# Performance work log

Measured on AMD Instinct MI355X. Metric: run time of the kernel, lower is better.

Reference implementation:

```python
import jax, jax.numpy as jnp
import numpy as np

B, T, E, H = 4, 1024, 512, 8


def setup_inputs() -> dict:
    key = jax.random.key(0)
    ks = jax.random.split(key, 8)
    s = 1.0 / np.sqrt(E)
    return {
        "x": jax.random.normal(ks[0], (B, T, E), dtype=jnp.float32),
        "mask": jnp.zeros((B, T, T), dtype=jnp.float32),
        "Wk": jax.random.uniform(ks[1], (H * E, E), minval=-s, maxval=s, dtype=jnp.float32),
        "Wq": jax.random.uniform(ks[2], (H * E, E), minval=-s, maxval=s, dtype=jnp.float32),
        "Wv": jax.random.uniform(ks[3], (H * E, E), minval=-s, maxval=s, dtype=jnp.float32),
        "Wu": jax.random.uniform(ks[4], (E, H * E), minval=-s, maxval=s, dtype=jnp.float32),
        "bu": jnp.zeros((E,), dtype=jnp.float32),
        "heads": H,
    }


def reference(x, mask, Wk, Wq, Wv, Wu, bu, heads):
    b, t, e = x.shape
    h = heads
    # Projections: torch Linear computes x @ W.T; output features laid out as [h, e]
    k = (x @ Wk.T).reshape(b, t, h, e).transpose(0, 2, 1, 3)  # [b,h,t,e]
    q = (x @ Wq.T).reshape(b, t, h, e).transpose(0, 2, 1, 3)
    v = (x @ Wv.T).reshape(b, t, h, e).transpose(0, 2, 1, 3)
    dot = jnp.einsum("bhqe,bhke->bhqk", q, k) / jnp.sqrt(jnp.float32(e))
    # mask repeat_interleave over b*h == broadcast over heads; subtracted additively
    att = jax.nn.softmax(dot - mask[:, None, :, :], axis=-1)
    out = jnp.einsum("bhqk,bhke->bhqe", att, v)  # [b,h,t,e]
    out = out.transpose(0, 2, 1, 3).reshape(b, t, h * e)
    return out @ Wu.T + bu
```

## Files before the change

kernel.cpp:

```cpp
#include <hip/hip_runtime.h>
#include <hip/hip_bf16.h>


typedef short bf16x8 __attribute__((ext_vector_type(8)));
typedef float f32x4 __attribute__((ext_vector_type(4)));
typedef unsigned short u16x8 __attribute__((ext_vector_type(8)));

__device__ __forceinline__ unsigned short f2bf(float f) {
  unsigned int u = __float_as_uint(f);
  u += 0x7FFFu + ((u >> 16) & 1u);
  return (unsigned short)(u >> 16);
}
__device__ __forceinline__ float bf2f(unsigned short s) {
  return __uint_as_float(((unsigned int)s) << 16);
}

typedef const __attribute__((address_space(1))) unsigned int* gas1_t;
typedef __attribute__((address_space(3))) unsigned int* las3_t;

__device__ __forceinline__ void gload16(const unsigned short* g, unsigned short* l) {
  __builtin_amdgcn_global_load_lds((gas1_t)g, (las3_t)l, 16, 0, 0);
}

__device__ __forceinline__ void store_val(unsigned short* p, float v) { *p = f2bf(v); }
__device__ __forceinline__ void store_val(float* p, float v) { *p = v; }

template<typename OutT>
__global__ __launch_bounds__(512, 1) void gemm_bt2(
    const unsigned short* __restrict__ A, const unsigned short* __restrict__ B,
    OutT* __restrict__ C,
    int K, int lda, int ldb, int ldc, int zshift,
    long long sAb, long long sAh, long long sBb, long long sBh,
    long long sCb, long long sCh, float alpha,
    const unsigned short* __restrict__ A2, const unsigned short* __restrict__ B2,
    OutT* __restrict__ C2, int lda2,
    long long sA2h, long long sB2h, long long sC2h, int selGE)
{
  const int tid  = threadIdx.x;
  const int lane = tid & 63;
  const int wave = tid >> 6;
  const int l15 = lane & 15, lhi = lane >> 4;
  const int wm = wave >> 2, wn = wave & 3;

  const int nx = gridDim.x, nxy = gridDim.x * gridDim.y;
  const int nwg = nxy * gridDim.z;
  int flat = blockIdx.x + nx * blockIdx.y + nxy * blockIdx.z;
  flat = (flat & 7) * (nwg >> 3) + (flat >> 3);
  const int bz = flat / nxy;
  const int rem = flat - bz * nxy;
  const int by = rem / nx;
  const int bx = rem - by * nx;

  const int bb = bz >> zshift, hh = bz & ((1 << zshift) - 1);
  const long long m0 = (long long)by * 256;
  const long long n0 = (long long)bx * 256;

  const unsigned short* Ab;
  const unsigned short* Bb;
  OutT* Cb;
  int ldaU = lda;
  if (selGE >= 0 && hh >= selGE) {
    const int h2 = hh - selGE;
    Ab = A2 + (size_t)h2 * sA2h;
    Bb = B2 + (size_t)h2 * sB2h;
    Cb = C2 + (size_t)h2 * sC2h;
    ldaU = lda2;
  } else {
    Ab = A + bb * sAb + hh * sAh;
    Bb = B + bb * sBb + hh * sBh;
    Cb = C + bb * sCb + hh * sCh;
  }

  __shared__ __align__(16) unsigned short lds[49152];

  const unsigned short* gA[2];
  const unsigned short* gB[2];
  int fidx[2];
#pragma unroll
  for (int c = 0; c < 2; ++c) {
    const int f = c * 8 + wave;
    fidx[c] = f;
    gA[c] = Ab + (size_t)(m0 + f * 16 + l15) * ldaU + lhi * 8;
    gB[c] = Bb + (size_t)(n0 + f * 16 + l15) * ldb + lhi * 8;
  }

  auto stage = [&](int n, int p) {
    unsigned short* dst = lds + p * 16384;
    const int ko = n * 32;
#pragma unroll
    for (int c = 0; c < 2; ++c) {
      gload16(gA[c] + ko, dst + fidx[c] * 512);
      gload16(gB[c] + ko, dst + 8192 + fidx[c] * 512);
    }
  };

  f32x4 acc[8][4];
#pragma unroll
  for (int m = 0; m < 8; ++m)
#pragma unroll
    for (int n = 0; n < 4; ++n) acc[m][n] = (f32x4){0.f, 0.f, 0.f, 0.f};

  const int nt = K >> 5;
  stage(0, 0);
  stage(1, 1);
  asm volatile("s_waitcnt vmcnt(4)" ::: "memory");
  __builtin_amdgcn_sched_barrier(0);
  __builtin_amdgcn_s_barrier();

  for (int t = 0; t < nt; ++t) {
    const bool pref = (t + 2 < nt);
    if (pref) stage(t + 2, (t + 2) % 3);
    const unsigned short* base = lds + (t % 3) * 16384;
    bf16x8 af[8], bf[4];
#pragma unroll
    for (int mf = 0; mf < 8; ++mf)
      af[mf] = *(const bf16x8*)(base + (wm * 8 + mf) * 512 + lane * 8);
#pragma unroll
    for (int nf = 0; nf < 4; ++nf)
      bf[nf] = *(const bf16x8*)(base + 8192 + (wn * 4 + nf) * 512 + lane * 8);
    __builtin_amdgcn_s_setprio(1);
#pragma unroll
    for (int mf = 0; mf < 8; ++mf)
#pragma unroll
      for (int nf = 0; nf < 4; ++nf)
        acc[mf][nf] = __builtin_amdgcn_mfma_f32_16x16x32_bf16(af[mf], bf[nf], acc[mf][nf], 0, 0, 0);
    __builtin_amdgcn_s_setprio(0);
    if (pref) asm volatile("s_waitcnt vmcnt(4)" ::: "memory");
    else      asm volatile("s_waitcnt vmcnt(0)" ::: "memory");
    __builtin_amdgcn_sched_barrier(0);
    __builtin_amdgcn_s_barrier();
    __builtin_amdgcn_sched_barrier(0);
  }

#pragma unroll
  for (int mf = 0; mf < 8; ++mf) {
#pragma unroll
    for (int nf = 0; nf < 4; ++nf) {
      const long long col = n0 + wn * 64 + nf * 16 + l15;
#pragma unroll
      for (int r = 0; r < 4; ++r) {
        const long long row = m0 + wm * 128 + mf * 16 + lhi * 4 + r;
        store_val(Cb + (size_t)row * ldc + col, acc[mf][nf][r] * alpha);
      }
    }
  }
}

__global__ __launch_bounds__(256) void wtrans_kernel(
    const unsigned short* __restrict__ Wq, const unsigned short* __restrict__ Wk,
    const unsigned short* __restrict__ Wv,
    unsigned short* __restrict__ Wqt, unsigned short* __restrict__ Wkt,
    unsigned short* __restrict__ Wvt)
{
  __shared__ unsigned short t[64][72];
  const int k0 = blockIdx.x * 64;
  const int i0 = blockIdx.y * 64;
  const int hz = blockIdx.z;
  const int h = hz & 7;
  const int w = hz >> 3;
  const unsigned short* src = (w == 0) ? Wq : ((w == 1) ? Wk : Wv);
  unsigned short* dst = (w == 0) ? Wqt : ((w == 1) ? Wkt : Wvt);
  const int tid = threadIdx.x;
  const int r = tid >> 2, c16 = (tid & 3) * 16;
  const unsigned short* sp = src + (size_t)(h * 512 + k0 + r) * 512 + i0 + c16;
  u16x8 v0 = *(const u16x8*)sp;
  u16x8 v1 = *(const u16x8*)(sp + 8);
#pragma unroll
  for (int j = 0; j < 8; ++j) { t[r][c16 + j] = v0[j]; t[r][c16 + 8 + j] = v1[j]; }
  __syncthreads();
  unsigned short o[16];
#pragma unroll
  for (int j = 0; j < 16; ++j) o[j] = t[c16 + j][r];
  unsigned short* dp = dst + (size_t)h * 262144 + (size_t)(i0 + r) * 512 + k0 + c16;
  *(u16x8*)dp = *(u16x8*)o;
  *(u16x8*)(dp + 8) = *(u16x8*)(o + 8);
}

__global__ __launch_bounds__(256) void reduce_kernel(
    const float* __restrict__ P, const float* __restrict__ bias,
    float* __restrict__ out)
{
  const int i = blockIdx.x * 256 + threadIdx.x;
  const int col4 = i & 127;
  const float4* p4 = (const float4*)P + i;
  float4 s = p4[0];
#pragma unroll
  for (int z = 1; z < 8; ++z) {
    float4 v = p4[(size_t)z * 524288];
    s.x += v.x; s.y += v.y; s.z += v.z; s.w += v.w;
  }
  float4 b = ((const float4*)bias)[col4];
  s.x += b.x; s.y += b.y; s.z += b.z; s.w += b.w;
  ((float4*)out)[i] = s;
}

__global__ __launch_bounds__(256) void cast5_kernel(
    const float* __restrict__ s0, const float* __restrict__ s1,
    const float* __restrict__ s2, const float* __restrict__ s3,
    const float* __restrict__ s4, unsigned short* __restrict__ dst)
{
  const int seg = blockIdx.x >> 11;
  const int off = (blockIdx.x & 2047) * 256 + threadIdx.x;
  const float* s = s0;
  if (seg == 1) s = s1; else if (seg == 2) s = s2;
  else if (seg == 3) s = s3; else if (seg == 4) s = s4;
  float4 v = ((const float4*)s)[off];
  ushort4 o;
  o.x = f2bf(v.x); o.y = f2bf(v.y); o.z = f2bf(v.z); o.w = f2bf(v.w);
  ((ushort4*)dst)[(size_t)seg * 524288 + off] = o;
}

__global__ __launch_bounds__(256) void softmax_kernel(
    unsigned short* __restrict__ S, const float* __restrict__ mask)
{
  const int wave = threadIdx.x >> 6;
  const int lane = threadIdx.x & 63;
  const long long row = (long long)blockIdx.x * 4 + wave;
  const int q = (int)(row & 1023);
  const int b = (int)(row >> 13);
  unsigned short* Srow = S + row * 1024;
  const float* mrow = mask + ((size_t)b * 1024 + q) * 1024;

  u16x8 sv0 = ((const u16x8*)Srow)[lane * 2];
  u16x8 sv1 = ((const u16x8*)Srow)[lane * 2 + 1];
  float mk[16];
  const float4* m4 = (const float4*)mrow + lane * 4;
#pragma unroll
  for (int t = 0; t < 4; ++t) {
    float4 v = m4[t];
    mk[t * 4 + 0] = v.x; mk[t * 4 + 1] = v.y; mk[t * 4 + 2] = v.z; mk[t * 4 + 3] = v.w;
  }

  float lg[16];
#pragma unroll
  for (int j = 0; j < 8; ++j) lg[j] = bf2f(sv0[j]) - mk[j];
#pragma unroll
  for (int j = 0; j < 8; ++j) lg[8 + j] = bf2f(sv1[j]) - mk[8 + j];

  float mx = lg[0];
#pragma unroll
  for (int j = 1; j < 16; ++j) mx = fmaxf(mx, lg[j]);
#pragma unroll
  for (int off = 32; off > 0; off >>= 1) mx = fmaxf(mx, __shfl_xor(mx, off));

  float ex[16], sm = 0.f;
#pragma unroll
  for (int j = 0; j < 16; ++j) { ex[j] = __expf(lg[j] - mx); sm += ex[j]; }
#pragma unroll
  for (int off = 32; off > 0; off >>= 1) sm += __shfl_xor(sm, off);
  const float rinv = 1.0f / sm;

  u16x8 o0, o1;
#pragma unroll
  for (int j = 0; j < 8; ++j) o0[j] = f2bf(ex[j] * rinv);
#pragma unroll
  for (int j = 0; j < 8; ++j) o1[j] = f2bf(ex[8 + j] * rinv);
  ((u16x8*)Srow)[lane * 2] = o0;
  ((u16x8*)Srow)[lane * 2 + 1] = o1;
}

extern "C" void kernel_launch(void* const* d_in, const int* in_sizes, int n_in,
                              void* d_out, int out_size, void* d_ws, size_t ws_size,
                              hipStream_t stream) {
  const float* x    = (const float*)d_in[0];
  const float* mask = (const float*)d_in[1];
  const float* Wk   = (const float*)d_in[2];
  const float* Wq   = (const float*)d_in[3];
  const float* Wv   = (const float*)d_in[4];
  const float* Wu   = (const float*)d_in[5];
  const float* bu   = (const float*)d_in[6];

  const size_t MB = 1024 * 1024;
  if (ws_size < 192 * MB) return;
  char* ws = (char*)d_ws;
  unsigned short* xb  = (unsigned short*)(ws + 0 * MB);
  unsigned short* Wqb = (unsigned short*)(ws + 4 * MB);
  unsigned short* Wkb = (unsigned short*)(ws + 8 * MB);
  unsigned short* Wvb = (unsigned short*)(ws + 12 * MB);
  unsigned short* Wub = (unsigned short*)(ws + 16 * MB);
  unsigned short* Wqt = (unsigned short*)(ws + 20 * MB);
  unsigned short* Wkt = (unsigned short*)(ws + 24 * MB);
  unsigned short* Wvt = (unsigned short*)(ws + 28 * MB);
  unsigned short* Nh  = (unsigned short*)(ws + 32 * MB);
  unsigned short* Gh  = (unsigned short*)(ws + 36 * MB);
  unsigned short* xM  = (unsigned short*)(ws + 40 * MB);
  unsigned short* xGt = (unsigned short*)(ws + 72 * MB);
  unsigned short* Sb  = (unsigned short*)(ws + 104 * MB);
  float* Pk = (float*)(ws + 4 * MB);

  cast5_kernel<<<5 * 2048, 256, 0, stream>>>(x, Wq, Wk, Wv, Wu, xb);

  wtrans_kernel<<<dim3(8, 8, 24), 256, 0, stream>>>(Wqb, Wkb, Wvb, Wqt, Wkt, Wvt);

  gemm_bt2<unsigned short><<<dim3(2, 2, 16), 512, 0, stream>>>(
      Wkt, Wqt, Nh,
      512, 512, 512, 512, 4,
      0, 262144LL, 0, 262144LL, 0, 262144LL, 1.0f,
      Wub, Wvt, Gh, 4096, 512LL, 262144LL, 262144LL, 8);

  gemm_bt2<unsigned short><<<dim3(2, 16, 8), 512, 0, stream>>>(
      xb, Nh, xM,
      512, 512, 512, 4096, 0,
      0, 0, 262144LL, 0, 512LL, 0, 1.0f,
      nullptr, nullptr, nullptr, 0, 0, 0, 0, -1);

  gemm_bt2<unsigned short><<<dim3(16, 16, 1), 512, 0, stream>>>(
      Gh, xb, xGt,
      512, 512, 512, 4096, 0,
      0, 0, 0, 0, 0, 0, 1.0f,
      nullptr, nullptr, nullptr, 0, 0, 0, 0, -1);

  gemm_bt2<unsigned short><<<dim3(4, 4, 32), 512, 0, stream>>>(
      xM, xb, Sb,
      512, 4096, 512, 1024, 3,
      4194304LL, 512LL, 524288LL, 0, 8388608LL, 1048576LL,
      0.044194173824159216f,
      nullptr, nullptr, nullptr, 0, 0, 0, 0, -1);

  softmax_kernel<<<8192, 256, 0, stream>>>(Sb, mask);

  gemm_bt2<float><<<dim3(2, 4, 32), 512, 0, stream>>>(
      Sb, xGt, Pk,
      1024, 1024, 4096, 512, 3,
      8388608LL, 1048576LL, 1024LL, 2097152LL, 524288LL, 2097152LL, 1.0f,
      nullptr, nullptr, nullptr, 0, 0, 0, 0, -1);

  reduce_kernel<<<2048, 256, 0, stream>>>(Pk, bu, (float*)d_out);
}
```

Baseline: 224.7 us.

## Fuse weight cast into transpose, merge two GEMMs, share mask across heads in softmax

The fp32-to-bf16 cast of Wq/Wk/Wv moves into the transpose kernel, so the intermediate bf16 weight copies are no longer written and re-read. The xM and xGt GEMMs are merged into a single launch through the selGE dual-problem path, with m/n tile indices swapped for the second problem. The softmax kernel now runs one block per (batch, query) with eight waves, one per head, so each mask row is fetched by one block instead of by separate blocks per head. The workspace layout is reshuffled to match.

```diff
diff --git a/kernel.cpp b/kernel.cpp
--- a/kernel.cpp
+++ b/kernel.cpp
@@ -52,23 +52,26 @@
   const int bx = rem - by * nx;
 
   const int bb = bz >> zshift, hh = bz & ((1 << zshift) - 1);
-  const long long m0 = (long long)by * 256;
-  const long long n0 = (long long)bx * 256;
 
   const unsigned short* Ab;
   const unsigned short* Bb;
   OutT* Cb;
   int ldaU = lda;
+  long long m0, n0;
   if (selGE >= 0 && hh >= selGE) {
     const int h2 = hh - selGE;
     Ab = A2 + (size_t)h2 * sA2h;
     Bb = B2 + (size_t)h2 * sB2h;
     Cb = C2 + (size_t)h2 * sC2h;
     ldaU = lda2;
+    m0 = (long long)bx * 256;
+    n0 = (long long)by * 256;
   } else {
     Ab = A + bb * sAb + hh * sAh;
     Bb = B + bb * sBb + hh * sBh;
     Cb = C + bb * sCb + hh * sCh;
+    m0 = (long long)by * 256;
+    n0 = (long long)bx * 256;
   }
 
   __shared__ __align__(16) unsigned short lds[49152];
@@ -147,8 +150,8 @@
 }
 
 __global__ __launch_bounds__(256) void wtrans_kernel(
-    const unsigned short* __restrict__ Wq, const unsigned short* __restrict__ Wk,
-    const unsigned short* __restrict__ Wv,
+    const float* __restrict__ Wq, const float* __restrict__ Wk,
+    const float* __restrict__ Wv,
     unsigned short* __restrict__ Wqt, unsigned short* __restrict__ Wkt,
     unsigned short* __restrict__ Wvt)
 {
@@ -158,15 +161,19 @@
   const int hz = blockIdx.z;
   const int h = hz & 7;
   const int w = hz >> 3;
-  const unsigned short* src = (w == 0) ? Wq : ((w == 1) ? Wk : Wv);
+  const float* src = (w == 0) ? Wq : ((w == 1) ? Wk : Wv);
   unsigned short* dst = (w == 0) ? Wqt : ((w == 1) ? Wkt : Wvt);
   const int tid = threadIdx.x;
   const int r = tid >> 2, c16 = (tid & 3) * 16;
-  const unsigned short* sp = src + (size_t)(h * 512 + k0 + r) * 512 + i0 + c16;
-  u16x8 v0 = *(const u16x8*)sp;
-  u16x8 v1 = *(const u16x8*)(sp + 8);
-#pragma unroll
-  for (int j = 0; j < 8; ++j) { t[r][c16 + j] = v0[j]; t[r][c16 + 8 + j] = v1[j]; }
+  const float* sp = src + (size_t)(h * 512 + k0 + r) * 512 + i0 + c16;
+#pragma unroll
+  for (int g = 0; g < 4; ++g) {
+    float4 v = *(const float4*)(sp + g * 4);
+    t[r][c16 + g * 4 + 0] = f2bf(v.x);
+    t[r][c16 + g * 4 + 1] = f2bf(v.y);
+    t[r][c16 + g * 4 + 2] = f2bf(v.z);
+    t[r][c16 + g * 4 + 3] = f2bf(v.w);
+  }
   __syncthreads();
   unsigned short o[16];
 #pragma unroll
@@ -194,32 +201,29 @@
   ((float4*)out)[i] = s;
 }
 
-__global__ __launch_bounds__(256) void cast5_kernel(
+__global__ __launch_bounds__(256) void cast2_kernel(
     const float* __restrict__ s0, const float* __restrict__ s1,
-    const float* __restrict__ s2, const float* __restrict__ s3,
-    const float* __restrict__ s4, unsigned short* __restrict__ dst)
+    unsigned short* __restrict__ d0, unsigned short* __restrict__ d1)
 {
   const int seg = blockIdx.x >> 11;
   const int off = (blockIdx.x & 2047) * 256 + threadIdx.x;
-  const float* s = s0;
-  if (seg == 1) s = s1; else if (seg == 2) s = s2;
-  else if (seg == 3) s = s3; else if (seg == 4) s = s4;
+  const float* s = seg ? s1 : s0;
+  unsigned short* d = seg ? d1 : d0;
   float4 v = ((const float4*)s)[off];
   ushort4 o;
   o.x = f2bf(v.x); o.y = f2bf(v.y); o.z = f2bf(v.z); o.w = f2bf(v.w);
-  ((ushort4*)dst)[(size_t)seg * 524288 + off] = o;
-}
-
-__global__ __launch_bounds__(256) void softmax_kernel(
+  ((ushort4*)d)[off] = o;
+}
+
+__global__ __launch_bounds__(512) void softmax_kernel(
     unsigned short* __restrict__ S, const float* __restrict__ mask)
 {
   const int wave = threadIdx.x >> 6;
   const int lane = threadIdx.x & 63;
-  const long long row = (long long)blockIdx.x * 4 + wave;
-  const int q = (int)(row & 1023);
-  const int b = (int)(row >> 13);
-  unsigned short* Srow = S + row * 1024;
-  const float* mrow = mask + ((size_t)b * 1024 + q) * 1024;
+  const int bq = blockIdx.x;
+  const int b = bq >> 10, q = bq & 1023;
+  unsigned short* Srow = S + (((size_t)(b * 8 + wave)) * 1024 + q) * 1024;
+  const float* mrow = mask + ((size_t)(b * 1024 + q)) * 1024;
 
   u16x8 sv0 = ((const u16x8*)Srow)[lane * 2];
   u16x8 sv1 = ((const u16x8*)Srow)[lane * 2 + 1];
@@ -274,23 +278,20 @@
   if (ws_size < 192 * MB) return;
   char* ws = (char*)d_ws;
   unsigned short* xb  = (unsigned short*)(ws + 0 * MB);
-  unsigned short* Wqb = (unsigned short*)(ws + 4 * MB);
-  unsigned short* Wkb = (unsigned short*)(ws + 8 * MB);
-  unsigned short* Wvb = (unsigned short*)(ws + 12 * MB);
-  unsigned short* Wub = (unsigned short*)(ws + 16 * MB);
-  unsigned short* Wqt = (unsigned short*)(ws + 20 * MB);
-  unsigned short* Wkt = (unsigned short*)(ws + 24 * MB);
-  unsigned short* Wvt = (unsigned short*)(ws + 28 * MB);
-  unsigned short* Nh  = (unsigned short*)(ws + 32 * MB);
-  unsigned short* Gh  = (unsigned short*)(ws + 36 * MB);
-  unsigned short* xM  = (unsigned short*)(ws + 40 * MB);
-  unsigned short* xGt = (unsigned short*)(ws + 72 * MB);
-  unsigned short* Sb  = (unsigned short*)(ws + 104 * MB);
-  float* Pk = (float*)(ws + 4 * MB);
-
-  cast5_kernel<<<5 * 2048, 256, 0, stream>>>(x, Wq, Wk, Wv, Wu, xb);
-
-  wtrans_kernel<<<dim3(8, 8, 24), 256, 0, stream>>>(Wqb, Wkb, Wvb, Wqt, Wkt, Wvt);
+  unsigned short* xGt = (unsigned short*)(ws + 4 * MB);
+  unsigned short* Sb  = (unsigned short*)(ws + 36 * MB);
+  unsigned short* Wub = (unsigned short*)(ws + 100 * MB);
+  unsigned short* Wqt = (unsigned short*)(ws + 104 * MB);
+  unsigned short* Wkt = (unsigned short*)(ws + 108 * MB);
+  unsigned short* Wvt = (unsigned short*)(ws + 112 * MB);
+  unsigned short* Nh  = (unsigned short*)(ws + 116 * MB);
+  unsigned short* Gh  = (unsigned short*)(ws + 120 * MB);
+  unsigned short* xM  = (unsigned short*)(ws + 124 * MB);
+  float* Pk = (float*)(ws + 100 * MB);
+
+  cast2_kernel<<<2 * 2048, 256, 0, stream>>>(x, Wu, xb, Wub);
+
+  wtrans_kernel<<<dim3(8, 8, 24), 256, 0, stream>>>(Wq, Wk, Wv, Wqt, Wkt, Wvt);
 
   gemm_bt2<unsigned short><<<dim3(2, 2, 16), 512, 0, stream>>>(
       Wkt, Wqt, Nh,
@@ -298,17 +299,11 @@
       0, 262144LL, 0, 262144LL, 0, 262144LL, 1.0f,
       Wub, Wvt, Gh, 4096, 512LL, 262144LL, 262144LL, 8);
 
-  gemm_bt2<unsigned short><<<dim3(2, 16, 8), 512, 0, stream>>>(
+  gemm_bt2<unsigned short><<<dim3(2, 16, 16), 512, 0, stream>>>(
       xb, Nh, xM,
-      512, 512, 512, 4096, 0,
-      0, 0, 262144LL, 0, 512LL, 0, 1.0f,
-      nullptr, nullptr, nullptr, 0, 0, 0, 0, -1);
-
-  gemm_bt2<unsigned short><<<dim3(16, 16, 1), 512, 0, stream>>>(
-      Gh, xb, xGt,
-      512, 512, 512, 4096, 0,
-      0, 0, 0, 0, 0, 0, 1.0f,
-      nullptr, nullptr, nullptr, 0, 0, 0, 0, -1);
+      512, 512, 512, 4096, 4,
+      0, 0, 0, 262144LL, 0, 512LL, 1.0f,
+      Gh, xb, xGt, 512, 262144LL, 0, 2097152LL, 8);
 
   gemm_bt2<unsigned short><<<dim3(4, 4, 32), 512, 0, stream>>>(
       xM, xb, Sb,
@@ -317,7 +312,7 @@
       0.044194173824159216f,
       nullptr, nullptr, nullptr, 0, 0, 0, 0, -1);
 
-  softmax_kernel<<<8192, 256, 0, stream>>>(Sb, mask);
+  softmax_kernel<<<4096, 512, 0, stream>>>(Sb, mask);
 
   gemm_bt2<float><<<dim3(2, 4, 32), 512, 0, stream>>>(
       Sb, xGt, Pk,
```

Measured after the change: 217.5 us. -3.2%, faster.
